# Optimization experiments

Measured on AMD Instinct MI355X. Metric: run time of the kernel, lower is better.

Reference implementation:

```python
import jax, jax.numpy as jnp
import numpy as np

B, S, D, H = 2, 2048, 1024, 16
HD = D // H  # 64
EPS = 1e-8


def setup_inputs() -> dict:
    key = jax.random.key(0)
    ks = jax.random.split(key, 9)
    hidden_states = jax.random.normal(ks[0], (B, S, D), dtype=jnp.float32)
    # rotary tables: standard RoPE angles over half the head dim
    pos = jnp.arange(S, dtype=jnp.float32)[:, None]
    inv_freq = 1.0 / (10000.0 ** (jnp.arange(0, HD, 2, dtype=jnp.float32) / HD))  # [HD/2]
    ang = pos * inv_freq[None, :]  # [S, HD/2]
    sin = jnp.sin(ang)[None, None]  # [1,1,S,HD/2]
    cos = jnp.cos(ang)[None, None]
    s = 1.0 / np.sqrt(D)
    wq = jax.random.normal(ks[1], (D, D), dtype=jnp.float32) * s
    wk = jax.random.normal(ks[2], (D, D), dtype=jnp.float32) * s
    wv = jax.random.normal(ks[3], (D, D), dtype=jnp.float32) * s
    wo = jax.random.normal(ks[4], (D, D), dtype=jnp.float32) * s
    bo = jnp.zeros((D,), dtype=jnp.float32)
    scale = jnp.ones((D,), dtype=jnp.float32)
    return {"hidden_states": hidden_states, "sin": sin, "cos": cos,
            "wq": wq, "wk": wk, "wv": wv, "wo": wo, "bo": bo, "scale": scale}


def _heads(x):
    # [B,S,D] -> [B,H,S,HD]
    return x.reshape(B, S, H, HD).transpose(0, 2, 1, 3)


def _rotary(x, sin, cos):
    # interleaved RoPE: even/odd pairs
    x1, x2 = x[..., 0::2], x[..., 1::2]
    out = jnp.stack([x1 * cos - x2 * sin, x2 * cos + x1 * sin], axis=-1)
    return out.reshape(x.shape)


def reference(hidden_states, sin, cos, wq, wk, wv, wo, bo, scale):
    q = _rotary(_heads(hidden_states @ wq.T), sin, cos)
    k = _rotary(_heads(hidden_states @ wk.T), sin, cos)
    v = _rotary(_heads(hidden_states @ wv.T), sin, cos)
    scores = jnp.einsum("bhqd,bhkd->bhqk", q, k) / np.sqrt(HD)
    probs = jax.nn.softmax(scores, axis=-1)
    ctx = jnp.einsum("bhqk,bhkd->bhqd", probs, v)
    ctx = ctx.transpose(0, 2, 1, 3).reshape(B, S, D)
    out = ctx @ wo.T + bo
    x = out + hidden_states
    # RMSNorm: x / (||x||/sqrt(d) + eps) * scale
    rms = jnp.linalg.norm(x, axis=-1, keepdims=True) / np.sqrt(D)
    return scale * (x / (rms + EPS))
```

## Files before the change

### kernel.cpp

```cpp
#include <hip/hip_runtime.h>
#include <cmath>

#define BB 2
#define SS 2048
#define DD 1024
#define HH 16
#define HDIM 64
#define KDIM 1024
#define EPSF 1e-8f
#define QSCALE 0.18033688f

typedef __attribute__((ext_vector_type(8))) short bf16x8;
typedef __attribute__((ext_vector_type(4))) float f32x4;
typedef __attribute__((ext_vector_type(16))) float f32x16;

__device__ __forceinline__ ushort f2bf(float x) {
    unsigned u = __builtin_bit_cast(unsigned, x);
    u += 0x7FFFu + ((u >> 16) & 1u);
    return (ushort)(u >> 16);
}

__device__ __forceinline__ unsigned pack_bf16_trunc(float a, float b) {
    return __builtin_amdgcn_perm(__builtin_bit_cast(unsigned, b),
                                 __builtin_bit_cast(unsigned, a), 0x07060302u);
}

__device__ __forceinline__ float exp2_fast(float x) {
    float r;
    asm("v_exp_f32 %0, %1" : "=v"(r) : "v"(x));
    return r;
}

__device__ __forceinline__ void gload_lds16(const ushort* g, ushort* l) {
    __builtin_amdgcn_global_load_lds(
        (const __attribute__((address_space(1))) unsigned*)g,
        (__attribute__((address_space(3))) unsigned*)l, 16, 0, 0);
}

__global__ __launch_bounds__(256) void conv_all(
    const float* __restrict__ hs, const float* __restrict__ wq,
    const float* __restrict__ wk, const float* __restrict__ wv,
    const float* __restrict__ wo, ushort* __restrict__ dst)
{
    const int i = blockIdx.x * 256 + threadIdx.x;
    const int HS4 = (BB * SS * DD) / 4;
    const int W4 = (DD * DD) / 4;
    const float* src;
    int off;
    if (i < HS4) { src = hs; off = i; }
    else {
        const int j = i - HS4;
        const int seg = j / W4;
        off = j - seg * W4;
        src = (seg == 0) ? wq : (seg == 1) ? wk : (seg == 2) ? wv : wo;
    }
    const float4 v = ((const float4*)src)[off];
    ushort4 o;
    o.x = f2bf(v.x); o.y = f2bf(v.y); o.z = f2bf(v.z); o.w = f2bf(v.w);
    ((ushort4*)dst)[i] = o;
}

__global__ __launch_bounds__(256) void gemm_qkv_mfma(
    const ushort* __restrict__ A,
    const ushort* __restrict__ Wq, const ushort* __restrict__ Wk,
    const ushort* __restrict__ Wv,
    const float* __restrict__ sinp, const float* __restrict__ cosp,
    ushort* __restrict__ Qb, ushort* __restrict__ Kb, ushort* __restrict__ Vtb)
{
    const int wg  = blockIdx.x;
    const int xcd = wg & 7, s = wg >> 3;
    const int pg  = xcd >> 2, rg = xcd & 3;
    const int cb  = pg * 12 + (s >> 3);
    const int row0 = (rg * 8 + (s & 7)) * 128;
    const int z = cb >> 3;
    const int col0 = (cb & 7) * 128;
    const ushort* W = (z == 0) ? Wq : (z == 1) ? Wk : Wv;
    ushort* O = (z == 0) ? Qb : (z == 1) ? Kb : Vtb;
    const float qs = (z == 0) ? QSCALE : 1.0f;

    __shared__ __align__(16) ushort As[128 * 32];
    __shared__ __align__(16) ushort Bs[128 * 32];

    const int tid = threadIdx.x;
    const int w = tid >> 6, lane = tid & 63;
    const int quad = lane >> 4, l15 = lane & 15;
    const int m_off = (w >> 1) * 64, n_off = (w & 1) * 64;

    f32x4 acc[4][4] = {};

    for (int k0 = 0; k0 < KDIM; k0 += 32) {
#pragma unroll
        for (int it = 0; it < 2; ++it) {
            const int L = (it * 4 + w) * 64 + lane;
            const int r = L >> 2, c8 = (L & 3) * 8;
            gload_lds16(A + (size_t)(row0 + r) * KDIM + k0 + c8, &As[L * 8]);
            gload_lds16(W + (size_t)(col0 + r) * KDIM + k0 + c8, &Bs[L * 8]);
        }
        __syncthreads();
        bf16x8 af[4], bfr[4];
#pragma unroll
        for (int i = 0; i < 4; ++i) {
            af[i]  = *(const bf16x8*)&As[(m_off + i * 16 + l15) * 32 + quad * 8];
            bfr[i] = *(const bf16x8*)&Bs[(n_off + i * 16 + l15) * 32 + quad * 8];
        }
#pragma unroll
        for (int i = 0; i < 4; ++i)
#pragma unroll
            for (int j = 0; j < 4; ++j)
                acc[i][j] = __builtin_amdgcn_mfma_f32_16x16x32_bf16(
                    af[i], bfr[j], acc[i][j], 0, 0, 0);
        __syncthreads();
    }

    const int b = (row0 + m_off) / SS;
#pragma unroll
    for (int mi = 0; mi < 4; ++mi) {
        const int mrow = row0 + m_off + mi * 16 + quad * 4;
#pragma unroll
        for (int ni = 0; ni < 4; ++ni) {
            const int c = col0 + n_off + ni * 16 + l15;
            const int h = c >> 6, e = c & 63;
            const int bh = b * HH + h;
            float outv[4];
#pragma unroll
            for (int r = 0; r < 4; ++r) {
                const int s2 = (mrow + r) & (SS - 1);
                const float sv = sinp[s2 * (HDIM / 2) + (e >> 1)];
                const float cv = cosp[s2 * (HDIM / 2) + (e >> 1)];
                const float v = acc[mi][ni][r];
                const float vp = __shfl_xor(v, 1);
                outv[r] = ((l15 & 1) ? (v * cv + vp * sv) : (v * cv - vp * sv)) * qs;
            }
            if (z < 2) {
#pragma unroll
                for (int r = 0; r < 4; ++r) {
                    const int s2 = (mrow + r) & (SS - 1);
                    const ushort mine = f2bf(outv[r]);
                    const ushort part = (ushort)__shfl_xor((int)mine, 1);
                    if (!(l15 & 1))
                        *(unsigned*)(O + ((size_t)(bh * SS + s2)) * HDIM + e) =
                            (unsigned)mine | ((unsigned)part << 16);
                }
            } else {
                ushort4 pk;
                pk.x = f2bf(outv[0]); pk.y = f2bf(outv[1]);
                pk.z = f2bf(outv[2]); pk.w = f2bf(outv[3]);
                const int s0 = mrow & (SS - 1);
                *(ushort4*)(O + ((size_t)(bh * HDIM + e)) * SS + s0) = pk;
            }
        }
    }
}

__global__ __launch_bounds__(256, 2) void attn_mfma(
    const ushort* __restrict__ Qb, const ushort* __restrict__ Kb,
    const ushort* __restrict__ Vtb, ushort* __restrict__ ctx)
{
    const int wg  = blockIdx.x;
    const int lin = (wg & 7) * 64 + (wg >> 3);
    const int bh   = lin >> 4;
    const int qblk = lin & 15;
    const int b = bh / HH, h = bh % HH;
    const int q0 = qblk * 128;
    const int tid = threadIdx.x;
    const int w = tid >> 6;
    const int lane = tid & 63;
    const int l31 = lane & 31;
    const int g = lane >> 5;
    const int strip = w >> 1;
    const int phase = w & 1;

    __shared__ __align__(16) ushort kvb[2][2][2][64][32];

    const ushort* Qh = Qb  + (size_t)bh * SS * HDIM;
    const ushort* Kh = Kb  + (size_t)bh * SS * HDIM;
    const ushort* Vh = Vtb + (size_t)bh * HDIM * SS;

    const int qrowA = q0 + strip * 64 + l31;
    const int qrowB = qrowA + 32;
    bf16x8 qf[2][4];
#pragma unroll
    for (int ks = 0; ks < 4; ++ks) {
        qf[0][ks] = *(const bf16x8*)(Qh + (size_t)qrowA * HDIM + ks * 16 + g * 8);
        qf[1][ks] = *(const bf16x8*)(Qh + (size_t)qrowB * HDIM + ks * 16 + g * 8);
    }

    f32x16 cacc[2][2] = {};
    float ls0a = 0.f, ls0b = 0.f, ls1a = 0.f, ls1b = 0.f;

    const int lr = lane >> 2;
    const int c16 = lane & 3;
    const int lc = c16 * 8;
    const int swc = (c16 ^ ((lr >> 1) & 3)) * 8;
    const int srow = w * 16 + lr;
    const int rsw = (l31 >> 1) & 3;

    uint4 rk0, rk1, rv0, rv1;

#define LOAD_STAGE(K0)                                                        \
    do {                                                                      \
        const ushort* Kp = Kh + (size_t)((K0) + srow) * HDIM + lc;            \
        const ushort* Vp = Vh + (size_t)srow * SS + (K0) + lc;                \
        rk0 = *(const uint4*)(Kp);                                            \
        rk1 = *(const uint4*)(Kp + 32);                                       \
        rv0 = *(const uint4*)(Vp);                                            \
        rv1 = *(const uint4*)(Vp + 32);                                       \
    } while (0)

#define WRITE_STAGE(bufi)                                                     \
    do {                                                                      \
        *(uint4*)&kvb[bufi][0][0][srow][swc] = rk0;                           \
        *(uint4*)&kvb[bufi][0][1][srow][swc] = rk1;                           \
        *(uint4*)&kvb[bufi][1][0][srow][swc] = rv0;                           \
        *(uint4*)&kvb[bufi][1][1][srow][swc] = rv1;                           \
    } while (0)

    const int NT = SS / 64;

    LOAD_STAGE(0);
    WRITE_STAGE(0);
    LOAD_STAGE(64);

    for (int t = 0; t < NT; ++t) {
        __syncthreads();
        const int cur = t & 1;

        bf16x8 kf[4];
#pragma unroll
        for (int ks = 0; ks < 4; ++ks)
            kf[ks] = *(const bf16x8*)&kvb[cur][0][ks >> 1]
                [phase * 32 + l31][(((ks & 1) * 2 + g) ^ rsw) * 8];

        if (t + 1 < NT) WRITE_STAGE(cur ^ 1);
        if (t + 2 < NT) LOAD_STAGE((t + 2) * 64);

        f32x16 sacc0 = {}, sacc1 = {};
        __builtin_amdgcn_s_setprio(1);
#pragma unroll
        for (int ks = 0; ks < 4; ++ks) {
            sacc0 = __builtin_amdgcn_mfma_f32_32x32x16_bf16(
                kf[ks], qf[0][ks], sacc0, 0, 0, 0);
            sacc1 = __builtin_amdgcn_mfma_f32_32x32x16_bf16(
                kf[ks], qf[1][ks], sacc1, 0, 0, 0);
        }
        __builtin_amdgcn_s_setprio(0);

        unsigned pk[2][8];
#pragma unroll
        for (int i = 0; i < 8; ++i) {
            const float pa0 = exp2_fast(sacc0[2 * i]);
            const float pb0 = exp2_fast(sacc0[2 * i + 1]);
            const float pa1 = exp2_fast(sacc1[2 * i]);
            const float pb1 = exp2_fast(sacc1[2 * i + 1]);
            if (i & 1) { ls0b += pa0 + pb0; ls1b += pa1 + pb1; }
            else       { ls0a += pa0 + pb0; ls1a += pa1 + pb1; }
            pk[0][i] = pack_bf16_trunc(pa0, pb0);
            pk[1][i] = pack_bf16_trunc(pa1, pb1);
        }

#pragma unroll
        for (int ks = 0; ks < 2; ++ks) {
            const int bq = ks * 4;
            unsigned a00 = pk[0][bq + 0], a01 = pk[0][bq + 1];
            unsigned b00 = pk[0][bq + 2], b01 = pk[0][bq + 3];
            unsigned a10 = pk[1][bq + 0], a11 = pk[1][bq + 1];
            unsigned b10 = pk[1][bq + 2], b11 = pk[1][bq + 3];
            asm("v_permlane32_swap_b32 %0, %1" : "+v"(a00), "+v"(b00));
            asm("v_permlane32_swap_b32 %0, %1" : "+v"(a01), "+v"(b01));
            asm("v_permlane32_swap_b32 %0, %1" : "+v"(a10), "+v"(b10));
            asm("v_permlane32_swap_b32 %0, %1" : "+v"(a11), "+v"(b11));
            union { unsigned u[4]; bf16x8 v; } pf0, pf1;
            pf0.u[0] = a00; pf0.u[1] = a01; pf0.u[2] = b00; pf0.u[3] = b01;
            pf1.u[0] = a10; pf1.u[1] = a11; pf1.u[2] = b10; pf1.u[3] = b11;
            __builtin_amdgcn_s_setprio(1);
#pragma unroll
            for (int dt = 0; dt < 2; ++dt) {
                const bf16x8 vf = *(const bf16x8*)&kvb[cur][1][phase]
                    [dt * 32 + l31][((ks * 2 + g) ^ rsw) * 8];
                cacc[0][dt] = __builtin_amdgcn_mfma_f32_32x32x16_bf16(
                    vf, pf0.v, cacc[0][dt], 0, 0, 0);
                cacc[1][dt] = __builtin_amdgcn_mfma_f32_32x32x16_bf16(
                    vf, pf1.v, cacc[1][dt], 0, 0, 0);
            }
            __builtin_amdgcn_s_setprio(0);
        }
    }

    float lsq[2];
    lsq[0] = ls0a + ls0b;
    lsq[1] = ls1a + ls1b;
    lsq[0] += __shfl_xor(lsq[0], 32);
    lsq[1] += __shfl_xor(lsq[1], 32);

    float* mlds = (float*)kvb;
    const int mbase = strip * 2112 + lane * 33;
#pragma unroll
    for (int qs = 0; qs < 2; ++qs) {
        __syncthreads();
        if (phase == 1) {
#pragma unroll
            for (int dt = 0; dt < 2; ++dt)
#pragma unroll
                for (int i = 0; i < 16; ++i)
                    mlds[mbase + dt * 16 + i] = cacc[qs][dt][i];
            mlds[mbase + 32] = lsq[qs];
        }
        __syncthreads();
        if (phase == 0) {
            f32x16 cf[2];
#pragma unroll
            for (int dt = 0; dt < 2; ++dt)
#pragma unroll
                for (int i = 0; i < 16; ++i)
                    cf[dt][i] = cacc[qs][dt][i] + mlds[mbase + dt * 16 + i];
            const float inv = 1.f / (lsq[qs] + mlds[mbase + 32]);

            const int qrow = (qs == 0) ? qrowA : qrowB;
            const size_t obase = ((size_t)(b * SS + qrow)) * DD + h * HDIM;
#pragma unroll
            for (int dt = 0; dt < 2; ++dt)
#pragma unroll
                for (int tt = 0; tt < 4; ++tt) {
                    ushort4 o;
                    o.x = f2bf(cf[dt][tt * 4 + 0] * inv);
                    o.y = f2bf(cf[dt][tt * 4 + 1] * inv);
                    o.z = f2bf(cf[dt][tt * 4 + 2] * inv);
                    o.w = f2bf(cf[dt][tt * 4 + 3] * inv);
                    *(ushort4*)(ctx + obase + dt * 32 + tt * 8 + g * 4) = o;
                }
        }
    }
#undef LOAD_STAGE
#undef WRITE_STAGE
}

__global__ __launch_bounds__(256) void gemm_out_mfma(
    const ushort* __restrict__ A, const ushort* __restrict__ W,
    const float* __restrict__ bias, float* __restrict__ Out)
{
    const int row0 = blockIdx.x * 128;
    const int col0 = blockIdx.y * 64;

    __shared__ __align__(16) ushort As[128 * 32];
    __shared__ __align__(16) ushort Bs[64 * 32];

    const int tid = threadIdx.x;
    const int w = tid >> 6, lane = tid & 63;
    const int quad = lane >> 4, l15 = lane & 15;
    const int m_off = (w >> 1) * 64, n_off = (w & 1) * 32;

    f32x4 acc[4][2] = {};

    for (int k0 = 0; k0 < KDIM; k0 += 32) {
#pragma unroll
        for (int it = 0; it < 2; ++it) {
            const int L = (it * 4 + w) * 64 + lane;
            const int r = L >> 2, c8 = (L & 3) * 8;
            gload_lds16(A + (size_t)(row0 + r) * KDIM + k0 + c8, &As[L * 8]);
        }
        {
            const int L = w * 64 + lane;
            const int r = L >> 2, c8 = (L & 3) * 8;
            gload_lds16(W + (size_t)(col0 + r) * KDIM + k0 + c8, &Bs[L * 8]);
        }
        __syncthreads();
        bf16x8 af[4], bfr[2];
#pragma unroll
        for (int i = 0; i < 4; ++i)
            af[i] = *(const bf16x8*)&As[(m_off + i * 16 + l15) * 32 + quad * 8];
#pragma unroll
        for (int j = 0; j < 2; ++j)
            bfr[j] = *(const bf16x8*)&Bs[(n_off + j * 16 + l15) * 32 + quad * 8];
#pragma unroll
        for (int i = 0; i < 4; ++i)
#pragma unroll
            for (int j = 0; j < 2; ++j)
                acc[i][j] = __builtin_amdgcn_mfma_f32_16x16x32_bf16(
                    af[i], bfr[j], acc[i][j], 0, 0, 0);
        __syncthreads();
    }

#pragma unroll
    for (int mi = 0; mi < 4; ++mi) {
        const int mrow = row0 + m_off + mi * 16 + quad * 4;
#pragma unroll
        for (int ni = 0; ni < 2; ++ni) {
            const int c = col0 + n_off + ni * 16 + l15;
            const float bv = bias[c];
#pragma unroll
            for (int r = 0; r < 4; ++r)
                Out[(size_t)(mrow + r) * DD + c] = acc[mi][ni][r] + bv;
        }
    }
}

__global__ __launch_bounds__(256) void resid_rmsnorm(
    const float* __restrict__ proj, const float* __restrict__ hs,
    const float* __restrict__ scale, float* __restrict__ out)
{
    const int t = blockIdx.x;
    const int tid = threadIdx.x;
    const size_t base = (size_t)t * DD + tid * 4;

    const float4 p4 = *(const float4*)(proj + base);
    const float4 h4 = *(const float4*)(hs + base);
    float x0 = p4.x + h4.x, x1 = p4.y + h4.y, x2 = p4.z + h4.z, x3 = p4.w + h4.w;
    float ss = x0 * x0 + x1 * x1 + x2 * x2 + x3 * x3;

#pragma unroll
    for (int off = 1; off < 64; off <<= 1) ss += __shfl_xor(ss, off);

    __shared__ float wsum[4];
    if ((tid & 63) == 0) wsum[tid >> 6] = ss;
    __syncthreads();
    const float total = wsum[0] + wsum[1] + wsum[2] + wsum[3];
    const float inv = 1.f / (sqrtf(total * (1.f / DD)) + EPSF);

    const float4 s4 = *(const float4*)(scale + tid * 4);
    float4 o;
    o.x = s4.x * x0 * inv;
    o.y = s4.y * x1 * inv;
    o.z = s4.z * x2 * inv;
    o.w = s4.w * x3 * inv;
    *(float4*)(out + base) = o;
}

extern "C" void kernel_launch(void* const* d_in, const int* in_sizes, int n_in,
                              void* d_out, int out_size, void* d_ws, size_t ws_size,
                              hipStream_t stream) {
    const float* hs    = (const float*)d_in[0];
    const float* sinp  = (const float*)d_in[1];
    const float* cosp  = (const float*)d_in[2];
    const float* wq    = (const float*)d_in[3];
    const float* wk    = (const float*)d_in[4];
    const float* wv    = (const float*)d_in[5];
    const float* wo    = (const float*)d_in[6];
    const float* bo    = (const float*)d_in[7];
    const float* scale = (const float*)d_in[8];
    float* out = (float*)d_out;

    unsigned char* wsb = (unsigned char*)d_ws;
    const size_t MAT = (size_t)BB * SS * DD;
    const size_t WN  = (size_t)DD * DD;
    ushort* Abf = (ushort*)wsb;
    ushort* Wqb = Abf + MAT;
    ushort* Wkb = Wqb + WN;
    ushort* Wvb = Wkb + WN;
    ushort* Wob = Wvb + WN;
    ushort* Qb  = Wob + WN;
    ushort* Kb  = Qb + MAT;
    ushort* Vtb = Kb + MAT;
    ushort* ctxb = Vtb + MAT;
    float* proj = (float*)(ctxb + MAT);

    const int nconv4 = (int)((MAT + 4 * WN) / 4);
    conv_all<<<dim3(nconv4 / 256), 256, 0, stream>>>(hs, wq, wk, wv, wo, Abf);

    gemm_qkv_mfma<<<dim3(768), 256, 0, stream>>>(Abf, Wqb, Wkb, Wvb,
                                                 sinp, cosp, Qb, Kb, Vtb);
    attn_mfma<<<dim3(512), 256, 0, stream>>>(Qb, Kb, Vtb, ctxb);
    gemm_out_mfma<<<dim3(32, 16), 256, 0, stream>>>(ctxb, Wob, bo, proj);
    resid_rmsnorm<<<dim3(BB * SS), 256, 0, stream>>>(proj, hs, scale, out);
}
```

Baseline: 196.4 us.

## Split attention key range in halves and merge partial contexts in new kernel

Attention now runs 1024 workgroups, each covering half of the key sequence for a 128-query block, and writes fp32 partial context plus a row-sum to workspace. A new merge kernel adds the two partials, normalizes, and converts to bf16 for the output projection. The aim is more parallelism and better occupancy on the attention stage, at the cost of extra fp32 traffic and one more launch. Merging by plain summation is only correct because no max subtraction is used, so both halves share the same exponent base.

```diff
diff --git a/kernel.cpp b/kernel.cpp
--- a/kernel.cpp
+++ b/kernel.cpp
@@ -154,12 +154,16 @@
 
 __global__ __launch_bounds__(256, 2) void attn_mfma(
     const ushort* __restrict__ Qb, const ushort* __restrict__ Kb,
-    const ushort* __restrict__ Vtb, ushort* __restrict__ ctx)
+    const ushort* __restrict__ Vtb, float* __restrict__ ctxp,
+    float* __restrict__ lsump)
 {
     const int wg  = blockIdx.x;
-    const int lin = (wg & 7) * 64 + (wg >> 3);
-    const int bh   = lin >> 4;
-    const int qblk = lin & 15;
+    const int lin = (wg & 7) * 128 + (wg >> 3);
+    const int bh    = lin >> 5;
+    const int rest  = lin & 31;
+    const int qblk  = rest >> 1;
+    const int khalf = rest & 1;
+    const int kbase = khalf * (SS / 2);
     const int b = bh / HH, h = bh % HH;
     const int q0 = qblk * 128;
     const int tid = threadIdx.x;
@@ -215,11 +219,11 @@
         *(uint4*)&kvb[bufi][1][1][srow][swc] = rv1;                           \
     } while (0)
 
-    const int NT = SS / 64;
-
-    LOAD_STAGE(0);
+    const int NT = (SS / 2) / 64;
+
+    LOAD_STAGE(kbase);
     WRITE_STAGE(0);
-    LOAD_STAGE(64);
+    LOAD_STAGE(kbase + 64);
 
     for (int t = 0; t < NT; ++t) {
         __syncthreads();
@@ -232,7 +236,7 @@
                 [phase * 32 + l31][(((ks & 1) * 2 + g) ^ rsw) * 8];
 
         if (t + 1 < NT) WRITE_STAGE(cur ^ 1);
-        if (t + 2 < NT) LOAD_STAGE((t + 2) * 64);
+        if (t + 2 < NT) LOAD_STAGE(kbase + (t + 2) * 64);
 
         f32x16 sacc0 = {}, sacc1 = {};
         __builtin_amdgcn_s_setprio(1);
@@ -313,25 +317,53 @@
 #pragma unroll
                 for (int i = 0; i < 16; ++i)
                     cf[dt][i] = cacc[qs][dt][i] + mlds[mbase + dt * 16 + i];
-            const float inv = 1.f / (lsq[qs] + mlds[mbase + 32]);
+            const float lt = lsq[qs] + mlds[mbase + 32];
 
             const int qrow = (qs == 0) ? qrowA : qrowB;
-            const size_t obase = ((size_t)(b * SS + qrow)) * DD + h * HDIM;
+            const size_t obase = (size_t)khalf * (BB * SS * DD)
+                               + ((size_t)(b * SS + qrow)) * DD + h * HDIM;
 #pragma unroll
             for (int dt = 0; dt < 2; ++dt)
 #pragma unroll
                 for (int tt = 0; tt < 4; ++tt) {
-                    ushort4 o;
-                    o.x = f2bf(cf[dt][tt * 4 + 0] * inv);
-                    o.y = f2bf(cf[dt][tt * 4 + 1] * inv);
-                    o.z = f2bf(cf[dt][tt * 4 + 2] * inv);
-                    o.w = f2bf(cf[dt][tt * 4 + 3] * inv);
-                    *(ushort4*)(ctx + obase + dt * 32 + tt * 8 + g * 4) = o;
+                    float4 o;
+                    o.x = cf[dt][tt * 4 + 0];
+                    o.y = cf[dt][tt * 4 + 1];
+                    o.z = cf[dt][tt * 4 + 2];
+                    o.w = cf[dt][tt * 4 + 3];
+                    *(float4*)(ctxp + obase + dt * 32 + tt * 8 + g * 4) = o;
                 }
+            if (g == 0)
+                lsump[(size_t)khalf * (BB * HH * SS) + (size_t)bh * SS + qrow] = lt;
         }
     }
 #undef LOAD_STAGE
 #undef WRITE_STAGE
+}
+
+__global__ __launch_bounds__(256) void merge_ctx(
+    const float* __restrict__ ctxp, const float* __restrict__ lsump,
+    ushort* __restrict__ ctx)
+{
+    const int t = blockIdx.x;
+    const int tid = threadIdx.x;
+    const int b = t >> 11, s = t & (SS - 1);
+    const int h = tid >> 4;
+    const int bh = b * HH + h;
+    const size_t base = (size_t)t * DD + tid * 4;
+
+    const float l0 = lsump[(size_t)bh * SS + s];
+    const float l1 = lsump[(size_t)(BB * HH) * SS + (size_t)bh * SS + s];
+    const float inv = 1.f / (l0 + l1);
+
+    const float4 c0 = *(const float4*)(ctxp + base);
+    const float4 c1 = *(const float4*)(ctxp + (size_t)(BB * SS * DD) + base);
+    ushort4 o;
+    o.x = f2bf((c0.x + c1.x) * inv);
+    o.y = f2bf((c0.y + c1.y) * inv);
+    o.z = f2bf((c0.z + c1.z) * inv);
+    o.w = f2bf((c0.w + c1.w) * inv);
+    *(ushort4*)(ctx + base) = o;
 }
 
 __global__ __launch_bounds__(256) void gemm_out_mfma(
@@ -452,13 +484,16 @@
     ushort* Vtb = Kb + MAT;
     ushort* ctxb = Vtb + MAT;
     float* proj = (float*)(ctxb + MAT);
+    float* ctxp = proj + MAT;
+    float* lsump = ctxp + 2 * MAT;
 
     const int nconv4 = (int)((MAT + 4 * WN) / 4);
     conv_all<<<dim3(nconv4 / 256), 256, 0, stream>>>(hs, wq, wk, wv, wo, Abf);
 
     gemm_qkv_mfma<<<dim3(768), 256, 0, stream>>>(Abf, Wqb, Wkb, Wvb,
                                                  sinp, cosp, Qb, Kb, Vtb);
-    attn_mfma<<<dim3(512), 256, 0, stream>>>(Qb, Kb, Vtb, ctxb);
+    attn_mfma<<<dim3(1024), 256, 0, stream>>>(Qb, Kb, Vtb, ctxp, lsump);
+    merge_ctx<<<dim3(BB * SS), 256, 0, stream>>>(ctxp, lsump, ctxb);
     gemm_out_mfma<<<dim3(32, 16), 256, 0, stream>>>(ctxb, Wob, bo, proj);
     resid_rmsnorm<<<dim3(BB * SS), 256, 0, stream>>>(proj, hs, scale, out);
 }
```

New measurement: 206.8 us. +5.3%, slower.
